# Performance work log

Measured on AMD Instinct MI355X. Metric: run time of the kernel, lower is better.

The kernel has to match this reference:

```python
import jax, jax.numpy as jnp
import numpy as np

N = 100000   # nodes
E = 300000   # directed edges
NG = 4096    # graphs in batch
F_IN = 22
HID = 128


def setup_inputs() -> dict:
    key = jax.random.key(0)
    ks = jax.random.split(key, 32)
    s = 0.05
    inp = {
        "x": jax.random.normal(ks[0], (N, F_IN), jnp.float32),
        "edge_index": jax.random.randint(ks[1], (2, E), 0, N),
        "batch": jnp.sort(jax.random.randint(ks[2], (N,), 0, NG)),
        # GAT layer 1: 22 -> 4 heads x 32
        "W1": jax.random.normal(ks[3], (F_IN, HID), jnp.float32) * s,
        "as1": jax.random.normal(ks[4], (4, 32), jnp.float32) * s,
        "ad1": jax.random.normal(ks[5], (4, 32), jnp.float32) * s,
        "b1": jnp.zeros((HID,), jnp.float32),
        "g1": jnp.ones((HID,), jnp.float32),
        "be1": jnp.zeros((HID,), jnp.float32),
        # GAT layer 2: 128 -> 4 heads x 32
        "W2": jax.random.normal(ks[6], (HID, HID), jnp.float32) * s,
        "as2": jax.random.normal(ks[7], (4, 32), jnp.float32) * s,
        "ad2": jax.random.normal(ks[8], (4, 32), jnp.float32) * s,
        "b2": jnp.zeros((HID,), jnp.float32),
        "g2": jnp.ones((HID,), jnp.float32),
        "be2": jnp.zeros((HID,), jnp.float32),
        # GAT layer 3: 128 -> 1 head x 128
        "W3": jax.random.normal(ks[9], (HID, HID), jnp.float32) * s,
        "as3": jax.random.normal(ks[10], (1, HID), jnp.float32) * s,
        "ad3": jax.random.normal(ks[11], (1, HID), jnp.float32) * s,
        "b3": jnp.zeros((HID,), jnp.float32),
        "g3": jnp.ones((HID,), jnp.float32),
        "be3": jnp.zeros((HID,), jnp.float32),
        # MLP head
        "fw1": jax.random.normal(ks[12], (HID, 64), jnp.float32) * s,
        "fb1": jnp.zeros((64,), jnp.float32),
        "fw2": jax.random.normal(ks[13], (64, 1), jnp.float32) * s,
        "fb2": jnp.zeros((1,), jnp.float32),
    }
    return inp


def reference(x, edge_index, batch, W1, as1, ad1, b1, g1, be1,
              W2, as2, ad2, b2, g2, be2, W3, as3, ad3, b3, g3, be3,
              fw1, fb1, fw2, fb2):
    n = x.shape[0]
    sl = jnp.arange(n)
    src = jnp.concatenate([edge_index[0], sl])  # PyG GATConv adds self-loops
    dst = jnp.concatenate([edge_index[1], sl])

    def gat(h_in, W, a_s, a_d, b):
        H, C = a_s.shape
        h = (h_in @ W).reshape(n, H, C)                      # [N,H,C]
        al_s = jnp.einsum('nhc,hc->nh', h, a_s)              # per-node src score
        al_d = jnp.einsum('nhc,hc->nh', h, a_d)
        e = jax.nn.leaky_relu(al_s[src] + al_d[dst], 0.2)    # [Etot,H]
        emax = jax.ops.segment_max(e, dst, num_segments=n)
        ex = jnp.exp(e - emax[dst])
        den = jax.ops.segment_sum(ex, dst, num_segments=n)
        alpha = ex / (den[dst] + 1e-16)                       # segment softmax over in-edges
        msg = h[src] * alpha[:, :, None]                      # [Etot,H,C]
        out = jax.ops.segment_sum(msg, dst, num_segments=n)
        return out.reshape(n, H * C) + b

    def bn(h, g, be):
        m = h.mean(0)
        v = h.var(0)
        return (h - m) * jax.lax.rsqrt(v + 1e-5) * g + be

    h = jax.nn.relu(bn(gat(x, W1, as1, ad1, b1), g1, be1))
    h = jax.nn.relu(bn(gat(h, W2, as2, ad2, b2), g2, be2))
    h = jax.nn.relu(bn(gat(h, W3, as3, ad3, b3), g3, be3))

    # global mean pool over graphs
    s = jax.ops.segment_sum(h, batch, num_segments=NG)
    cnt = jax.ops.segment_sum(jnp.ones((n,), h.dtype), batch, num_segments=NG)
    pooled = s / jnp.maximum(cnt, 1.0)[:, None]

    z = jax.nn.relu(pooled @ fw1 + fb1)
    return z @ fw2 + fb2
```

## Files before the change

kernel.cpp:

```cpp
#include <hip/hip_runtime.h>

#define N_NODES 100000
#define N_EDGES 300000
#define N_ETOT  400000
#define NGRAPH  4096
#define HID     128
#define NBLK_SCAN 391
#define PNPB    32
#define STATS_BLOCKS 512
#define NSLICE  64

typedef __attribute__((ext_vector_type(8))) short short8;
typedef __attribute__((ext_vector_type(8))) ushort ushort8;
typedef __attribute__((ext_vector_type(4))) float f32x4;

__device__ __forceinline__ ushort f2bf(float f) {
    union { float f; unsigned u; } x; x.f = f;
    unsigned r = x.u + 0x7FFF + ((x.u >> 16) & 1);
    return (ushort)(r >> 16);
}

__device__ __forceinline__ float bf2f(ushort v) {
    union { unsigned u; float f; } t;
    t.u = ((unsigned)v) << 16;
    return t.f;
}

__device__ __forceinline__ float2 bf2f2(unsigned v) {
    union { unsigned u; float f; } lo, hi;
    lo.u = v << 16;
    hi.u = v & 0xFFFF0000u;
    return make_float2(lo.f, hi.f);
}

__global__ __launch_bounds__(256) void setup_kernel(
    const float* __restrict__ x,
    const float* __restrict__ W1, const float* __restrict__ W2, const float* __restrict__ W3,
    ushort* __restrict__ Wt1, ushort* __restrict__ Wt2, ushort* __restrict__ Wt3,
    ushort* __restrict__ Xb, float* __restrict__ sums_sl, int* __restrict__ counts,
    float* __restrict__ pooled)
{
    const int i = blockIdx.x * 256 + threadIdx.x;
    if (i < 16384) {
        int c = i >> 7, k = i & 127;
        Wt2[c * 128 + k] = f2bf(W2[k * 128 + c]);
    } else if (i < 32768) {
        int j = i - 16384; int c = j >> 7, k = j & 127;
        Wt3[c * 128 + k] = f2bf(W3[k * 128 + c]);
    } else if (i < 36864) {
        int j = i - 32768; int c = j >> 5, k = j & 31;
        Wt1[c * 32 + k] = (k < 22) ? f2bf(W1[k * 128 + c]) : (ushort)0;
    } else if (i < 36864 + N_NODES * 32) {
        int j = i - 36864; int n = j >> 5, k = j & 31;
        Xb[j] = (k < 22) ? f2bf(x[n * 22 + k]) : (ushort)0;
    } else if (i < 36864 + N_NODES * 32 + NSLICE * 256) {
        sums_sl[i - (36864 + N_NODES * 32)] = 0.f;
    } else if (i < 36864 + N_NODES * 32 + NSLICE * 256 + N_NODES) {
        counts[i - (36864 + N_NODES * 32 + NSLICE * 256)] = 0;
    } else if (i < 36864 + N_NODES * 32 + NSLICE * 256 + N_NODES + NGRAPH * HID + NGRAPH) {
        pooled[i - (36864 + N_NODES * 32 + NSLICE * 256 + N_NODES)] = 0.f;
    }
}
#define SETUP_TOT (36864 + N_NODES * 32 + NSLICE * 256 + N_NODES + NGRAPH * HID + NGRAPH)

template<int K, bool PRE_BN, int HH>
__global__ __launch_bounds__(256) void mfma_gemm_kernel(
    const ushort* __restrict__ Ab, const ushort* __restrict__ Wt,
    const float* __restrict__ scale, const float* __restrict__ shift,
    const float* __restrict__ avs, const float* __restrict__ avd,
    ushort* __restrict__ Cb, float* __restrict__ als, float* __restrict__ ald, int M)
{
    constexpr int SEGS = K / 8;
    constexpr int SSH  = (K == 128) ? 4 : 2;
    constexpr int SWM  = SEGS - 1;
    constexpr int NP   = SEGS / 2;
    constexpr int KT   = K / 32;

    __shared__ ushort Asm[128 * K];
    __shared__ ushort Bsm[128 * K];

    const int tid  = threadIdx.x;
    const int wave = tid >> 6;
    const int lane = tid & 63;
    const int ln   = lane & 15;
    const int quad = lane >> 4;
    const int wr0  = (wave >> 1) * 64;
    const int wc0  = (wave & 1) * 64;
    const int row0 = blockIdx.x * 128;

    short8 aR[NP], wR[NP];
    #pragma unroll
    for (int q = 0; q < NP; ++q) {
        const int chunk = tid + q * 256;
        const int r   = chunk >> SSH;
        const int seg = chunk & SWM;
        aR[q] = *(const short8*)&Ab[(size_t)(row0 + r) * K + seg * 8];
        wR[q] = *(const short8*)&Wt[(size_t)r * K + seg * 8];
    }
    if constexpr (PRE_BN) {
        #pragma unroll
        for (int q = 0; q < NP; ++q) {
            const int seg = (tid + q * 256) & SWM;
            const int cc  = seg * 8;
            #pragma unroll
            for (int i = 0; i < 8; ++i) {
                float f = bf2f((ushort)aR[q][i]);
                f = fmaxf(f * scale[cc + i] + shift[cc + i], 0.f);
                aR[q][i] = (short)f2bf(f);
            }
        }
    }
    #pragma unroll
    for (int q = 0; q < NP; ++q) {
        const int chunk = tid + q * 256;
        const int r   = chunk >> SSH;
        const int seg = chunk & SWM;
        const int sp  = seg ^ (r & SWM);
        *(short8*)&Asm[r * K + sp * 8] = aR[q];
        *(short8*)&Bsm[r * K + sp * 8] = wR[q];
    }
    __syncthreads();

    f32x4 acc[4][4] = {};
    #pragma unroll
    for (int kt = 0; kt < KT; ++kt) {
        short8 af[4], bf[4];
        #pragma unroll
        for (int i = 0; i < 4; ++i) {
            const int ra = wr0 + i * 16 + ln;
            const int ca = wc0 + i * 16 + ln;
            af[i] = *(const short8*)&Asm[ra * K + (((kt * 4 + quad) ^ (ra & SWM)) * 8)];
            bf[i] = *(const short8*)&Bsm[ca * K + (((kt * 4 + quad) ^ (ca & SWM)) * 8)];
        }
        #pragma unroll
        for (int tr = 0; tr < 4; ++tr)
            #pragma unroll
            for (int tc = 0; tc < 4; ++tc)
                acc[tr][tc] = __builtin_amdgcn_mfma_f32_16x16x32_bf16(
                    af[tr], bf[tc], acc[tr][tc], 0, 0, 0);
    }

    #pragma unroll
    for (int tr = 0; tr < 4; ++tr)
        #pragma unroll
        for (int rg = 0; rg < 4; ++rg) {
            const int gr = row0 + wr0 + tr * 16 + quad * 4 + rg;
            if (gr < M) {
                #pragma unroll
                for (int tc = 0; tc < 4; ++tc)
                    Cb[(size_t)gr * HID + wc0 + tc * 16 + ln] = f2bf(acc[tr][tc][rg]);
            }
        }

    __syncthreads();
    float* ps = (float*)Asm;
    float* pd = (float*)Bsm;
    #pragma unroll
    for (int tr = 0; tr < 4; ++tr)
      #pragma unroll
      for (int rg = 0; rg < 4; ++rg) {
        float sA = 0.f, sB = 0.f, dA = 0.f, dB = 0.f;
        #pragma unroll
        for (int tc = 0; tc < 4; ++tc) {
            const int col = wc0 + tc * 16 + ln;
            const float v = acc[tr][tc][rg];
            if (tc < 2) { sA += v * avs[col]; dA += v * avd[col]; }
            else        { sB += v * avs[col]; dB += v * avd[col]; }
        }
        #pragma unroll
        for (int m = 1; m < 16; m <<= 1) {
            sA += __shfl_xor(sA, m); sB += __shfl_xor(sB, m);
            dA += __shfl_xor(dA, m); dB += __shfl_xor(dB, m);
        }
        if (ln == 0) {
            const int rl = wr0 + tr * 16 + quad * 4 + rg;
            const int h0 = (wave & 1) * 2;
            ps[rl * 4 + h0] = sA; ps[rl * 4 + h0 + 1] = sB;
            pd[rl * 4 + h0] = dA; pd[rl * 4 + h0 + 1] = dB;
        }
      }
    __syncthreads();
    {
        const int r  = tid & 127;
        const int gr = row0 + r;
        if (gr < M) {
            if (tid < 128) {
                if (HH == 4) {
                    #pragma unroll
                    for (int h = 0; h < 4; ++h) als[gr * 4 + h] = ps[r * 4 + h];
                } else als[gr] = ps[r * 4] + ps[r * 4 + 1] + ps[r * 4 + 2] + ps[r * 4 + 3];
            } else {
                if (HH == 4) {
                    #pragma unroll
                    for (int h = 0; h < 4; ++h) ald[gr * 4 + h] = pd[r * 4 + h];
                } else ald[gr] = pd[r * 4] + pd[r * 4 + 1] + pd[r * 4 + 2] + pd[r * 4 + 3];
            }
        }
    }
}

__global__ void hist_kernel(const int* __restrict__ ei, int* __restrict__ counts) {
    int e = blockIdx.x * blockDim.x + threadIdx.x;
    if (e >= N_ETOT) return;
    int dst = (e < N_EDGES) ? ei[N_EDGES + e] : e - N_EDGES;
    atomicAdd(&counts[dst], 1);
}

__global__ __launch_bounds__(256) void scanA_kernel(
    const int* __restrict__ counts, int* __restrict__ rowptr, int* __restrict__ bsum)
{
    __shared__ int ls[256];
    const int t = threadIdx.x;
    const int i = blockIdx.x * 256 + t;
    const int v = (i < N_NODES) ? counts[i] : 0;
    ls[t] = v; __syncthreads();
    #pragma unroll
    for (int off = 1; off < 256; off <<= 1) {
        int add = (t >= off) ? ls[t - off] : 0;
        __syncthreads();
        ls[t] += add;
        __syncthreads();
    }
    if (i < N_NODES) rowptr[i] = ls[t] - v;
    if (t == 255) bsum[blockIdx.x] = ls[255];
}

__global__ __launch_bounds__(512) void scanB_kernel(int* __restrict__ bsum)
{
    __shared__ int ls[512];
    const int t = threadIdx.x;
    const int v = (t < NBLK_SCAN) ? bsum[t] : 0;
    ls[t] = v; __syncthreads();
    #pragma unroll
    for (int off = 1; off < 512; off <<= 1) {
        int add = (t >= off) ? ls[t - off] : 0;
        __syncthreads();
        ls[t] += add;
        __syncthreads();
    }
    if (t < NBLK_SCAN) bsum[t] = ls[t] - v;
}

__global__ void scanC_kernel(int* __restrict__ rowptr, const int* __restrict__ bsum,
                             int* __restrict__ cursor)
{
    int i = blockIdx.x * 256 + threadIdx.x;
    if (i < N_NODES) {
        int v = rowptr[i] + bsum[blockIdx.x];
        rowptr[i] = v;
        cursor[i] = v;
    }
    if (i == 0) rowptr[N_NODES] = N_ETOT;
}

__global__ void scatter_kernel(const int* __restrict__ ei, int* __restrict__ cursor,
                               int* __restrict__ psrc)
{
    int e = blockIdx.x * blockDim.x + threadIdx.x;
    if (e >= N_ETOT) return;
    int src, dst;
    if (e < N_EDGES) { src = ei[e]; dst = ei[N_EDGES + e]; }
    else             { src = dst = e - N_EDGES; }
    int pos = atomicAdd(&cursor[dst], 1);
    psrc[pos] = src;
}

template<int HH>
__global__ __launch_bounds__(256) void agg_kernel(
    const ushort* __restrict__ H, const float* __restrict__ als,
    const float* __restrict__ ald, const int* __restrict__ rowptr,
    const int* __restrict__ psrc, ushort* __restrict__ Outb)
{
    const int tid  = threadIdx.x;
    const int node = blockIdx.x * 4 + (tid >> 6);
    const int lane = tid & 63;
    const int grp  = lane >> 4;
    const int cl   = lane & 15;
    const int hd   = (HH == 4) ? (cl >> 2) : 0;
    const int r0 = rowptr[node];
    const int r1 = rowptr[node + 1];
    const float aldh = (HH == 4) ? ald[node * 4 + hd] : ald[node];

    float den = 0.f;
    float acc[8] = {};
    for (int p = r0 + grp; p < r1; p += 4) {
        const int src = psrc[p];
        float v = ((HH == 4) ? als[src * 4 + hd] : als[src]) + aldh;
        v = (v > 0.f) ? v : 0.2f * v;
        const float ex = __expf(v);
        const uint4 hv = *(const uint4*)&H[(size_t)src * HID + cl * 8];
        const float2 h0 = bf2f2(hv.x), h1 = bf2f2(hv.y);
        const float2 h2 = bf2f2(hv.z), h3 = bf2f2(hv.w);
        acc[0] += ex * h0.x; acc[1] += ex * h0.y;
        acc[2] += ex * h1.x; acc[3] += ex * h1.y;
        acc[4] += ex * h2.x; acc[5] += ex * h2.y;
        acc[6] += ex * h3.x; acc[7] += ex * h3.y;
        den += ex;
    }
    #pragma unroll
    for (int m = 16; m < 64; m <<= 1) {
        den += __shfl_xor(den, m);
        #pragma unroll
        for (int i = 0; i < 8; ++i) acc[i] += __shfl_xor(acc[i], m);
    }
    if (grp == 0) {
        const float inv = 1.f / (den + 1e-16f);
        ushort8 o;
        #pragma unroll
        for (int i = 0; i < 8; ++i) o[i] = f2bf(acc[i] * inv);
        *(ushort8*)&Outb[(size_t)node * HID + cl * 8] = o;
    }
}

__global__ __launch_bounds__(256) void bn_stats_kernel(
    const ushort* __restrict__ X, float* __restrict__ sums_sl)
{
    __shared__ float ls[16][128], lq[16][128];
    const int tid = threadIdx.x;
    const int ro  = tid >> 4;
    const int ci  = tid & 15;
    const int c0  = ci * 8;
    const int rpb = (N_NODES + STATS_BLOCKS - 1) / STATS_BLOCKS;
    const int r0  = blockIdx.x * rpb;
    const int r1  = min(r0 + rpb, N_NODES);

    float s[8] = {}, q[8] = {};
    for (int r = r0 + ro; r < r1; r += 16) {
        const ushort8 v = *(const ushort8*)&X[(size_t)r * HID + c0];
        #pragma unroll
        for (int j = 0; j < 8; ++j) {
            const float f = bf2f(v[j]);
            s[j] += f; q[j] += f * f;
        }
    }
    #pragma unroll
    for (int j = 0; j < 8; ++j) { ls[ro][c0 + j] = s[j]; lq[ro][c0 + j] = q[j]; }
    __syncthreads();
    const int half = tid >> 7;
    const int c    = tid & 127;
    float acc = 0.f;
    if (half == 0) {
        #pragma unroll
        for (int k = 0; k < 16; ++k) acc += ls[k][c];
    } else {
        #pragma unroll
        for (int k = 0; k < 16; ++k) acc += lq[k][c];
    }
    atomicAdd(&sums_sl[(blockIdx.x & (NSLICE - 1)) * 256 + tid], acc);
}

__global__ __launch_bounds__(256) void bn_finalize_kernel(
    float* __restrict__ sums_sl,
    const float* __restrict__ g, const float* __restrict__ be,
    float* __restrict__ scale, float* __restrict__ shift)
{
    __shared__ float red[256];
    const int tid = threadIdx.x;
    float s = 0.f;
    for (int b = 0; b < NSLICE; ++b) {
        s += sums_sl[b * 256 + tid];
        sums_sl[b * 256 + tid] = 0.f;
    }
    red[tid] = s;
    __syncthreads();
    if (tid < 128) {
        const float m = red[tid] * (1.f / N_NODES);
        const float v = red[tid + 128] * (1.f / N_NODES) - m * m;
        const float sc = g[tid] * rsqrtf(v + 1e-5f);
        scale[tid] = sc;
        shift[tid] = be[tid] - m * sc;
    }
}

__global__ __launch_bounds__(128) void bn_pool_kernel(
    const ushort* __restrict__ X, const float* __restrict__ scale, const float* __restrict__ shift,
    const int* __restrict__ batch, float* __restrict__ pooled, float* __restrict__ cnt)
{
    const int c = threadIdx.x;
    const int n0 = blockIdx.x * PNPB;
    const int n1 = min(n0 + PNPB, N_NODES);
    const float sc = scale[c], sh = shift[c];
    int gcur = batch[n0];
    float acc = 0.f;
    int run = 0;
    for (int n = n0; n < n1; ++n) {
        const int g = batch[n];
        if (g != gcur) {
            atomicAdd(&pooled[(size_t)gcur * HID + c], acc);
            if (c == 0) atomicAdd(&cnt[gcur], (float)run);
            acc = 0.f; run = 0; gcur = g;
        }
        const float v = bf2f(X[(size_t)n * HID + c]) * sc + sh;
        acc += fmaxf(v, 0.f);
        ++run;
    }
    atomicAdd(&pooled[(size_t)gcur * HID + c], acc);
    if (c == 0) atomicAdd(&cnt[gcur], (float)run);
}

__global__ __launch_bounds__(256) void mlp_kernel(
    const float* __restrict__ pooled, const float* __restrict__ cnt,
    const float* __restrict__ fw1, const float* __restrict__ fb1,
    const float* __restrict__ fw2, const float* __restrict__ fb2,
    float* __restrict__ out)
{
    __shared__ float w1[HID * 64];
    __shared__ float rows[4][HID];
    const int tid = threadIdx.x;
    for (int i = tid; i < HID * 64; i += 256) w1[i] = fw1[i];
    const int gl = tid >> 6;
    const int j  = tid & 63;
    const float b1 = fb1[j];
    const float w2 = fw2[j];
    __syncthreads();
    #pragma unroll
    for (int it = 0; it < 4; ++it) {
        const int g = blockIdx.x * 16 + it * 4 + gl;
        const float inv = 1.f / fmaxf(cnt[g], 1.f);
        rows[gl][j]      = pooled[(size_t)g * HID + j] * inv;
        rows[gl][j + 64] = pooled[(size_t)g * HID + 64 + j] * inv;
        __syncthreads();
        float z = b1;
        #pragma unroll 8
        for (int c2 = 0; c2 < HID; ++c2) z += rows[gl][c2] * w1[c2 * 64 + j];
        z = fmaxf(z, 0.f);
        float p = z * w2;
        #pragma unroll
        for (int off = 32; off; off >>= 1) p += __shfl_down(p, off);
        if (j == 0) out[g] = p + fb2[0];
        __syncthreads();
    }
}

extern "C" void kernel_launch(void* const* d_in, const int* in_sizes, int n_in,
                              void* d_out, int out_size, void* d_ws, size_t ws_size,
                              hipStream_t stream)
{
    const float* x     = (const float*)d_in[0];
    const int*   ei    = (const int*)d_in[1];
    const int*   batch = (const int*)d_in[2];
    const float* W1  = (const float*)d_in[3];
    const float* as1 = (const float*)d_in[4];
    const float* ad1 = (const float*)d_in[5];
    const float* g1  = (const float*)d_in[7];
    const float* be1 = (const float*)d_in[8];
    const float* W2  = (const float*)d_in[9];
    const float* as2 = (const float*)d_in[10];
    const float* ad2 = (const float*)d_in[11];
    const float* g2  = (const float*)d_in[13];
    const float* be2 = (const float*)d_in[14];
    const float* W3  = (const float*)d_in[15];
    const float* as3 = (const float*)d_in[16];
    const float* ad3 = (const float*)d_in[17];
    const float* g3  = (const float*)d_in[19];
    const float* be3 = (const float*)d_in[20];
    const float* fw1 = (const float*)d_in[21];
    const float* fb1 = (const float*)d_in[22];
    const float* fw2 = (const float*)d_in[23];
    const float* fb2 = (const float*)d_in[24];
    float* out = (float*)d_out;

    ushort* Hb  = (ushort*)d_ws;
    ushort* Bh  = Hb  + (size_t)N_NODES * HID;
    ushort* Xb  = Bh  + (size_t)N_NODES * HID;
    ushort* Wt1 = Xb  + (size_t)N_NODES * 32;
    ushort* Wt2 = Wt1 + 128 * 32;
    ushort* Wt3 = Wt2 + 128 * 128;
    float* als    = (float*)(Wt3 + 128 * 128);
    float* ald    = als + (size_t)N_NODES * 4;
    float* sums_sl= ald + (size_t)N_NODES * 4;
    float* scale  = sums_sl + NSLICE * 256;
    float* shift  = scale + HID;
    float* pooled = shift + HID;
    float* cnt    = pooled + (size_t)NGRAPH * HID;
    int*   rowptr = (int*)(cnt + NGRAPH);
    int*   counts = rowptr + (N_NODES + 1);
    int*   cursor = counts + N_NODES;
    int*   bsum   = cursor + N_NODES;
    int*   psrc   = bsum + 512;

    auto cdiv = [](int a, int b) { return (a + b - 1) / b; };

    setup_kernel<<<cdiv(SETUP_TOT, 256), 256, 0, stream>>>(
        x, W1, W2, W3, Wt1, Wt2, Wt3, Xb, sums_sl, counts, pooled);

    hist_kernel<<<cdiv(N_ETOT, 256), 256, 0, stream>>>(ei, counts);
    scanA_kernel<<<NBLK_SCAN, 256, 0, stream>>>(counts, rowptr, bsum);
    scanB_kernel<<<1, 512, 0, stream>>>(bsum);
    scanC_kernel<<<NBLK_SCAN, 256, 0, stream>>>(rowptr, bsum, cursor);
    scatter_kernel<<<cdiv(N_ETOT, 256), 256, 0, stream>>>(ei, cursor, psrc);

    const int ggrid = cdiv(N_NODES, 128);
    const int agrid = N_NODES / 4;

    mfma_gemm_kernel<32, false, 4><<<ggrid, 256, 0, stream>>>(
        Xb, Wt1, nullptr, nullptr, as1, ad1, Hb, als, ald, N_NODES);
    agg_kernel<4><<<agrid, 256, 0, stream>>>(Hb, als, ald, rowptr, psrc, Bh);
    bn_stats_kernel<<<STATS_BLOCKS, 256, 0, stream>>>(Bh, sums_sl);
    bn_finalize_kernel<<<1, 256, 0, stream>>>(sums_sl, g1, be1, scale, shift);

    mfma_gemm_kernel<128, true, 4><<<ggrid, 256, 0, stream>>>(
        Bh, Wt2, scale, shift, as2, ad2, Hb, als, ald, N_NODES);
    agg_kernel<4><<<agrid, 256, 0, stream>>>(Hb, als, ald, rowptr, psrc, Bh);
    bn_stats_kernel<<<STATS_BLOCKS, 256, 0, stream>>>(Bh, sums_sl);
    bn_finalize_kernel<<<1, 256, 0, stream>>>(sums_sl, g2, be2, scale, shift);

    mfma_gemm_kernel<128, true, 1><<<ggrid, 256, 0, stream>>>(
        Bh, Wt3, scale, shift, as3, ad3, Hb, als, ald, N_NODES);
    agg_kernel<1><<<agrid, 256, 0, stream>>>(Hb, als, ald, rowptr, psrc, Bh);
    bn_stats_kernel<<<STATS_BLOCKS, 256, 0, stream>>>(Bh, sums_sl);
    bn_finalize_kernel<<<1, 256, 0, stream>>>(sums_sl, g3, be3, scale, shift);

    bn_pool_kernel<<<cdiv(N_NODES, PNPB), 128, 0, stream>>>(Bh, scale, shift, batch, pooled, cnt);
    mlp_kernel<<<NGRAPH / 16, 256, 0, stream>>>(pooled, cnt, fw1, fb1, fw2, fb2, out);
}
```

Measured before the change: 362.1 us.

## Fuse x conversion into GEMM, BN finalize into stats, drop scanB kernel

The first GEMM now reads float x directly and converts it to bf16 while loading, so the large Xb staging pass in setup is gone. The BN finalize step is folded into bn_stats through a last-block ticket counter with atomic loads, and scanB is removed by having each scanC block sum the preceding block totals itself. The goal is to cut four kernel launches and one full pass over the node features, at the cost of uncoalesced scalar loads of x and redundant prefix sums in every scanC block.

```diff
diff --git a/kernel.cpp b/kernel.cpp
--- a/kernel.cpp
+++ b/kernel.cpp
@@ -33,12 +33,20 @@
     return make_float2(lo.f, hi.f);
 }
 
+__device__ __forceinline__ float aload(const float* p) {
+    return __hip_atomic_load(p, __ATOMIC_RELAXED, __HIP_MEMORY_SCOPE_AGENT);
+}
+
+#define SETUP_W      36864
+#define SETUP_SUMS   (SETUP_W + NSLICE * 256)
+#define SETUP_CNTS   (SETUP_SUMS + N_NODES)
+#define SETUP_POOL   (SETUP_CNTS + NGRAPH * HID + NGRAPH)
+#define SETUP_TOT    (SETUP_POOL + 1)
 __global__ __launch_bounds__(256) void setup_kernel(
-    const float* __restrict__ x,
     const float* __restrict__ W1, const float* __restrict__ W2, const float* __restrict__ W3,
     ushort* __restrict__ Wt1, ushort* __restrict__ Wt2, ushort* __restrict__ Wt3,
-    ushort* __restrict__ Xb, float* __restrict__ sums_sl, int* __restrict__ counts,
-    float* __restrict__ pooled)
+    float* __restrict__ sums_sl, int* __restrict__ counts,
+    float* __restrict__ pooled, int* __restrict__ ticket)
 {
     const int i = blockIdx.x * 256 + threadIdx.x;
     if (i < 16384) {
@@ -47,25 +55,24 @@
     } else if (i < 32768) {
         int j = i - 16384; int c = j >> 7, k = j & 127;
         Wt3[c * 128 + k] = f2bf(W3[k * 128 + c]);
-    } else if (i < 36864) {
+    } else if (i < SETUP_W) {
         int j = i - 32768; int c = j >> 5, k = j & 31;
         Wt1[c * 32 + k] = (k < 22) ? f2bf(W1[k * 128 + c]) : (ushort)0;
-    } else if (i < 36864 + N_NODES * 32) {
-        int j = i - 36864; int n = j >> 5, k = j & 31;
-        Xb[j] = (k < 22) ? f2bf(x[n * 22 + k]) : (ushort)0;
-    } else if (i < 36864 + N_NODES * 32 + NSLICE * 256) {
-        sums_sl[i - (36864 + N_NODES * 32)] = 0.f;
-    } else if (i < 36864 + N_NODES * 32 + NSLICE * 256 + N_NODES) {
-        counts[i - (36864 + N_NODES * 32 + NSLICE * 256)] = 0;
-    } else if (i < 36864 + N_NODES * 32 + NSLICE * 256 + N_NODES + NGRAPH * HID + NGRAPH) {
-        pooled[i - (36864 + N_NODES * 32 + NSLICE * 256 + N_NODES)] = 0.f;
-    }
-}
-#define SETUP_TOT (36864 + N_NODES * 32 + NSLICE * 256 + N_NODES + NGRAPH * HID + NGRAPH)
-
-template<int K, bool PRE_BN, int HH>
+    } else if (i < SETUP_SUMS) {
+        sums_sl[i - SETUP_W] = 0.f;
+    } else if (i < SETUP_CNTS) {
+        counts[i - SETUP_SUMS] = 0;
+    } else if (i < SETUP_POOL) {
+        pooled[i - SETUP_CNTS] = 0.f;
+    } else if (i == SETUP_POOL) {
+        ticket[0] = 0;
+    }
+}
+
+template<int K, bool PRE_BN, int HH, bool DX>
 __global__ __launch_bounds__(256) void mfma_gemm_kernel(
-    const ushort* __restrict__ Ab, const ushort* __restrict__ Wt,
+    const ushort* __restrict__ Ab, const float* __restrict__ Af,
+    const ushort* __restrict__ Wt,
     const float* __restrict__ scale, const float* __restrict__ shift,
     const float* __restrict__ avs, const float* __restrict__ avd,
     ushort* __restrict__ Cb, float* __restrict__ als, float* __restrict__ ald, int M)
@@ -94,7 +101,17 @@
         const int chunk = tid + q * 256;
         const int r   = chunk >> SSH;
         const int seg = chunk & SWM;
-        aR[q] = *(const short8*)&Ab[(size_t)(row0 + r) * K + seg * 8];
+        if constexpr (DX) {
+            const int rr = min(row0 + r, N_NODES - 1);
+            #pragma unroll
+            for (int i = 0; i < 8; ++i) {
+                const int c = seg * 8 + i;
+                const float f = (c < 22) ? Af[(size_t)rr * 22 + c] : 0.f;
+                aR[q][i] = (short)f2bf(f);
+            }
+        } else {
+            aR[q] = *(const short8*)&Ab[(size_t)(row0 + r) * K + seg * 8];
+        }
         wR[q] = *(const short8*)&Wt[(size_t)r * K + seg * 8];
     }
     if constexpr (PRE_BN) {
@@ -225,28 +242,24 @@
     if (t == 255) bsum[blockIdx.x] = ls[255];
 }
 
-__global__ __launch_bounds__(512) void scanB_kernel(int* __restrict__ bsum)
-{
-    __shared__ int ls[512];
+__global__ __launch_bounds__(256) void scanC_kernel(
+    int* __restrict__ rowptr, const int* __restrict__ bsum, int* __restrict__ cursor)
+{
+    __shared__ int red[256];
     const int t = threadIdx.x;
-    const int v = (t < NBLK_SCAN) ? bsum[t] : 0;
-    ls[t] = v; __syncthreads();
-    #pragma unroll
-    for (int off = 1; off < 512; off <<= 1) {
-        int add = (t >= off) ? ls[t - off] : 0;
+    int s = 0;
+    for (int b = t; b < (int)blockIdx.x; b += 256) s += bsum[b];
+    red[t] = s;
+    __syncthreads();
+    #pragma unroll
+    for (int off = 128; off; off >>= 1) {
+        if (t < off) red[t] += red[t + off];
         __syncthreads();
-        ls[t] += add;
-        __syncthreads();
-    }
-    if (t < NBLK_SCAN) bsum[t] = ls[t] - v;
-}
-
-__global__ void scanC_kernel(int* __restrict__ rowptr, const int* __restrict__ bsum,
-                             int* __restrict__ cursor)
-{
-    int i = blockIdx.x * 256 + threadIdx.x;
+    }
+    const int base = red[0];
+    const int i = blockIdx.x * 256 + t;
     if (i < N_NODES) {
-        int v = rowptr[i] + bsum[blockIdx.x];
+        const int v = rowptr[i] + base;
         rowptr[i] = v;
         cursor[i] = v;
     }
@@ -313,7 +326,9 @@
 }
 
 __global__ __launch_bounds__(256) void bn_stats_kernel(
-    const ushort* __restrict__ X, float* __restrict__ sums_sl)
+    const ushort* __restrict__ X, float* __restrict__ sums_sl, int* __restrict__ ticket,
+    const float* __restrict__ g, const float* __restrict__ be,
+    float* __restrict__ scale, float* __restrict__ shift)
 {
     __shared__ float ls[16][128], lq[16][128];
     const int tid = threadIdx.x;
@@ -347,21 +362,22 @@
         for (int k = 0; k < 16; ++k) acc += lq[k][c];
     }
     atomicAdd(&sums_sl[(blockIdx.x & (NSLICE - 1)) * 256 + tid], acc);
-}
-
-__global__ __launch_bounds__(256) void bn_finalize_kernel(
-    float* __restrict__ sums_sl,
-    const float* __restrict__ g, const float* __restrict__ be,
-    float* __restrict__ scale, float* __restrict__ shift)
-{
+
+    __threadfence();
+    __shared__ int lastFlag;
+    __syncthreads();
+    if (tid == 0) lastFlag = (atomicAdd(ticket, 1) == STATS_BLOCKS - 1);
+    __syncthreads();
+    if (!lastFlag) return;
+
+    if (tid == 0) atomicExch(ticket, 0);
+    float t = 0.f;
+    for (int b = 0; b < NSLICE; ++b) {
+        t += aload(&sums_sl[b * 256 + tid]);
+        sums_sl[b * 256 + tid] = 0.f;
+    }
     __shared__ float red[256];
-    const int tid = threadIdx.x;
-    float s = 0.f;
-    for (int b = 0; b < NSLICE; ++b) {
-        s += sums_sl[b * 256 + tid];
-        sums_sl[b * 256 + tid] = 0.f;
-    }
-    red[tid] = s;
+    red[tid] = t;
     __syncthreads();
     if (tid < 128) {
         const float m = red[tid] * (1.f / N_NODES);
@@ -462,8 +478,7 @@
 
     ushort* Hb  = (ushort*)d_ws;
     ushort* Bh  = Hb  + (size_t)N_NODES * HID;
-    ushort* Xb  = Bh  + (size_t)N_NODES * HID;
-    ushort* Wt1 = Xb  + (size_t)N_NODES * 32;
+    ushort* Wt1 = Bh  + (size_t)N_NODES * HID + 128 * 128;
     ushort* Wt2 = Wt1 + 128 * 32;
     ushort* Wt3 = Wt2 + 128 * 128;
     float* als    = (float*)(Wt3 + 128 * 128);
@@ -478,38 +493,35 @@
     int*   cursor = counts + N_NODES;
     int*   bsum   = cursor + N_NODES;
     int*   psrc   = bsum + 512;
+    int*   ticket = psrc + N_ETOT;
 
     auto cdiv = [](int a, int b) { return (a + b - 1) / b; };
 
     setup_kernel<<<cdiv(SETUP_TOT, 256), 256, 0, stream>>>(
-        x, W1, W2, W3, Wt1, Wt2, Wt3, Xb, sums_sl, counts, pooled);
+        W1, W2, W3, Wt1, Wt2, Wt3, sums_sl, counts, pooled, ticket);
 
     hist_kernel<<<cdiv(N_ETOT, 256), 256, 0, stream>>>(ei, counts);
     scanA_kernel<<<NBLK_SCAN, 256, 0, stream>>>(counts, rowptr, bsum);
-    scanB_kernel<<<1, 512, 0, stream>>>(bsum);
     scanC_kernel<<<NBLK_SCAN, 256, 0, stream>>>(rowptr, bsum, cursor);
     scatter_kernel<<<cdiv(N_ETOT, 256), 256, 0, stream>>>(ei, cursor, psrc);
 
     const int ggrid = cdiv(N_NODES, 128);
     const int agrid = N_NODES / 4;
 
-    mfma_gemm_kernel<32, false, 4><<<ggrid, 256, 0, stream>>>(
-        Xb, Wt1, nullptr, nullptr, as1, ad1, Hb, als, ald, N_NODES);
+    mfma_gemm_kernel<32, false, 4, true><<<ggrid, 256, 0, stream>>>(
+        nullptr, x, Wt1, nullptr, nullptr, as1, ad1, Hb, als, ald, N_NODES);
     agg_kernel<4><<<agrid, 256, 0, stream>>>(Hb, als, ald, rowptr, psrc, Bh);
-    bn_stats_kernel<<<STATS_BLOCKS, 256, 0, stream>>>(Bh, sums_sl);
-    bn_finalize_kernel<<<1, 256, 0, stream>>>(sums_sl, g1, be1, scale, shift);
-
-    mfma_gemm_kernel<128, true, 4><<<ggrid, 256, 0, stream>>>(
-        Bh, Wt2, scale, shift, as2, ad2, Hb, als, ald, N_NODES);
+    bn_stats_kernel<<<STATS_BLOCKS, 256, 0, stream>>>(Bh, sums_sl, ticket, g1, be1, scale, shift);
+
+    mfma_gemm_kernel<128, true, 4, false><<<ggrid, 256, 0, stream>>>(
+        Bh, nullptr, Wt2, scale, shift, as2, ad2, Hb, als, ald, N_NODES);
     agg_kernel<4><<<agrid, 256, 0, stream>>>(Hb, als, ald, rowptr, psrc, Bh);
-    bn_stats_kernel<<<STATS_BLOCKS, 256, 0, stream>>>(Bh, sums_sl);
-    bn_finalize_kernel<<<1, 256, 0, stream>>>(sums_sl, g2, be2, scale, shift);
-
-    mfma_gemm_kernel<128, true, 1><<<ggrid, 256, 0, stream>>>(
-        Bh, Wt3, scale, shift, as3, ad3, Hb, als, ald, N_NODES);
+    bn_stats_kernel<<<STATS_BLOCKS, 256, 0, stream>>>(Bh, sums_sl, ticket, g2, be2, scale, shift);
+
+    mfma_gemm_kernel<128, true, 1, false><<<ggrid, 256, 0, stream>>>(
+        Bh, nullptr, Wt3, scale, shift, as3, ad3, Hb, als, ald, N_NODES);
     agg_kernel<1><<<agrid, 256, 0, stream>>>(Hb, als, ald, rowptr, psrc, Bh);
-    bn_stats_kernel<<<STATS_BLOCKS, 256, 0, stream>>>(Bh, sums_sl);
-    bn_finalize_kernel<<<1, 256, 0, stream>>>(sums_sl, g3, be3, scale, shift);
+    bn_stats_kernel<<<STATS_BLOCKS, 256, 0, stream>>>(Bh, sums_sl, ticket, g3, be3, scale, shift);
 
     bn_pool_kernel<<<cdiv(N_NODES, PNPB), 128, 0, stream>>>(Bh, scale, shift, batch, pooled, cnt);
     mlp_kernel<<<NGRAPH / 16, 256, 0, stream>>>(pooled, cnt, fw1, fb1, fw2, fb2, out);
```

After: 503.0 us. +38.9%, slower.
